# Kernel tuning notes

Hardware: AMD Instinct MI355X
Metric: run time of the kernel (lower is better)

## Reference

```python
import jax, jax.numpy as jnp
import numpy as np

D_MODEL = 1024
N_HEADS = 16
HEAD_DIM = D_MODEL // N_HEADS


def setup_inputs() -> dict:
    key = jax.random.key(0)
    ks = jax.random.split(key, 9)
    s = 1.0 / np.sqrt(D_MODEL)
    mk = lambda k: jax.random.uniform(k, (D_MODEL, D_MODEL), jnp.float32, -s, s)
    mb = lambda k: jax.random.uniform(k, (D_MODEL,), jnp.float32, -s, s)
    return {
        "x": jax.random.normal(ks[0], (2, 2048, D_MODEL), jnp.float32),
        "Wq": mk(ks[1]), "bq": mb(ks[2]),
        "Wk": mk(ks[3]), "bk": mb(ks[4]),
        "Wv": mk(ks[5]), "bv": mb(ks[6]),
        "Wo": mk(ks[7]), "bo": mb(ks[8]),
    }


def _split_heads(t, B, S):
    # [B,S,D] -> [B,H,S,hd]
    return t.reshape(B, S, N_HEADS, HEAD_DIM).transpose(0, 2, 1, 3)


def reference(x, Wq, bq, Wk, bk, Wv, bv, Wo, bo):
    B, S, _ = x.shape
    # torch Linear: y = x @ W.T + b  (W stored [out, in])
    Q = _split_heads(x @ Wq.T + bq, B, S)
    K = _split_heads(x @ Wk.T + bk, B, S)
    V = _split_heads(x @ Wv.T + bv, B, S)
    scores = jnp.einsum("bhsd,bhtd->bhst", Q, K) / np.sqrt(HEAD_DIM).astype(np.float32)
    attn = jax.nn.softmax(scores, axis=-1)
    out = jnp.einsum("bhst,bhtd->bhsd", attn, V)
    out = out.transpose(0, 2, 1, 3).reshape(B, S, D_MODEL)
    return out @ Wo.T + bo
```

## Files before the change

kernel.cpp:

```cpp
#include <hip/hip_runtime.h>
#include <math.h>

#define D_MODEL 1024
#define NH 16
#define HD 64
#define SEQ 2048
#define NB 2
#define BSROWS (NB * SEQ)
#define NT (SEQ / 64)

typedef __attribute__((ext_vector_type(8)))  short short8;
typedef __attribute__((ext_vector_type(4)))  float f32x4;
typedef __attribute__((ext_vector_type(16))) float f32x16;

__device__ __forceinline__ ushort bf16rne(float f) {
    union { float f; uint32_t u; } v; v.f = f;
    return (ushort)((v.u + 0x7FFFu + ((v.u >> 16) & 1u)) >> 16);
}

__device__ __forceinline__ void gl_lds16(const void* g, void* l) {
    __builtin_amdgcn_global_load_lds(
        reinterpret_cast<const uint32_t __attribute__((address_space(1)))*>(
            reinterpret_cast<uintptr_t>(g)),
        reinterpret_cast<uint32_t __attribute__((address_space(3)))*>(
            reinterpret_cast<uintptr_t>(l)),
        16, 0, 0);
}

__global__ __launch_bounds__(256) void convert_x(const float* __restrict__ in,
                                                 ushort* __restrict__ out) {
    const int i = blockIdx.x * 256 + threadIdx.x;
    const float4 a = ((const float4*)in)[2 * i];
    const float4 b = ((const float4*)in)[2 * i + 1];
    union { ushort u[8]; uint4 v; } r;
    r.u[0] = bf16rne(a.x); r.u[1] = bf16rne(a.y); r.u[2] = bf16rne(a.z); r.u[3] = bf16rne(a.w);
    r.u[4] = bf16rne(b.x); r.u[5] = bf16rne(b.y); r.u[6] = bf16rne(b.z); r.u[7] = bf16rne(b.w);
    ((uint4*)out)[i] = r.v;
}

__global__ __launch_bounds__(256) void convert_w(const float* __restrict__ w0,
                                                 const float* __restrict__ w1,
                                                 const float* __restrict__ w2,
                                                 const float* __restrict__ w3,
                                                 ushort* __restrict__ qkv,
                                                 ushort* __restrict__ wo) {
    const int which = blockIdx.y;
    const float* src = (which == 0) ? w0 : (which == 1) ? w1 : (which == 2) ? w2 : w3;
    ushort* dst = (which < 3) ? (qkv + (size_t)which * D_MODEL * D_MODEL) : wo;
    const int i = blockIdx.x * 256 + threadIdx.x;
    const float4 a = ((const float4*)src)[2 * i];
    const float4 b = ((const float4*)src)[2 * i + 1];
    union { ushort u[8]; uint4 v; } r;
    r.u[0] = bf16rne(a.x); r.u[1] = bf16rne(a.y); r.u[2] = bf16rne(a.z); r.u[3] = bf16rne(a.w);
    r.u[4] = bf16rne(b.x); r.u[5] = bf16rne(b.y); r.u[6] = bf16rne(b.z); r.u[7] = bf16rne(b.w);
    ((uint4*)dst)[i] = r.v;
}

template <int BN, int MODE>
__global__ __launch_bounds__(256) void gemm_mfma(const ushort* __restrict__ A,
                                                 const ushort* __restrict__ B,
                                                 const float* __restrict__ b0,
                                                 const float* __restrict__ b1,
                                                 const float* __restrict__ b2,
                                                 void* __restrict__ o0v,
                                                 void* __restrict__ o1v,
                                                 void* __restrict__ o2v) {
    constexpr int BM = 128, BK = 32;
    constexpr int WN = (BN == 128) ? 64 : 32;
    constexpr int NM = 4;
    constexpr int NN = WN / 16;

    __shared__ ushort As[BM * BK];
    __shared__ ushort Bs[BN * BK];

    const int tid = threadIdx.x;
    const int w   = tid >> 6;
    const int l   = tid & 63;
    const int i0  = blockIdx.x * BM;
    const int n0  = blockIdx.y * BN;

    const int wr = (w >> 1) * 64;
    const int wc = (w & 1) * WN;

    const int srow = l >> 2;
    const int scol = (l & 3) * 8;
    const ushort* ga = A + (size_t)(i0 + w * 32 + srow) * D_MODEL + scol;
    const ushort* gb = B + (size_t)(n0 + w * (BN / 4) + srow) * D_MODEL + scol;
    ushort* lA = &As[(w * 32) * BK];
    ushort* lB = &Bs[(w * (BN / 4)) * BK];

    f32x4 acc[NM][NN];
#pragma unroll
    for (int m = 0; m < NM; ++m)
#pragma unroll
        for (int n = 0; n < NN; ++n) acc[m][n] = (f32x4){0.f, 0.f, 0.f, 0.f};

    const int fr = l & 15;
    const int kc = (l >> 4) * 8;

    for (int k0 = 0; k0 < D_MODEL; k0 += BK) {
        __syncthreads();
        gl_lds16(ga, lA);
        gl_lds16(ga + 16 * D_MODEL, lA + 16 * BK);
        gl_lds16(gb, lB);
        if (BN == 128) gl_lds16(gb + 16 * D_MODEL, lB + 16 * BK);
        ga += BK; gb += BK;
        __syncthreads();

        short8 af[NM], bfr[NN];
#pragma unroll
        for (int m = 0; m < NM; ++m)
            af[m] = *(const short8*)&As[(wr + m * 16 + fr) * BK + kc];
#pragma unroll
        for (int n = 0; n < NN; ++n)
            bfr[n] = *(const short8*)&Bs[(wc + n * 16 + fr) * BK + kc];
#pragma unroll
        for (int m = 0; m < NM; ++m)
#pragma unroll
            for (int n = 0; n < NN; ++n)
                acc[m][n] = __builtin_amdgcn_mfma_f32_16x16x32_bf16(af[m], bfr[n], acc[m][n], 0, 0, 0);
    }

    const int rr = (l >> 4) * 4;

    if (MODE == 1) {
        float* out = (float*)o0v;
#pragma unroll
        for (int n = 0; n < NN; ++n) {
            const int j = n0 + wc + n * 16 + fr;
            const float bj = b0[j];
#pragma unroll
            for (int m = 0; m < NM; ++m) {
                const int row = i0 + wr + m * 16 + rr;
#pragma unroll
                for (int r = 0; r < 4; ++r)
                    out[(size_t)(row + r) * D_MODEL + j] = acc[m][n][r] + bj;
            }
        }
    } else {
        const int p = n0 >> 10;
        const float* bias = (p == 0) ? b0 : (p == 1) ? b1 : b2;
        const float scl = (p == 0) ? 0.125f : 1.0f;
#pragma unroll
        for (int n = 0; n < NN; ++n) {
            const int j = n0 + wc + n * 16 + fr;
            const int f = j & 1023;
            const float bj = bias[f];
            const int h = f >> 6, d = f & 63;
#pragma unroll
            for (int m = 0; m < NM; ++m) {
                const int row = i0 + wr + m * 16 + rr;
                const int bb = row >> 11;
                const int s0 = row & (SEQ - 1);
                if (p < 2) {
                    ushort* dst = (ushort*)(p == 0 ? o0v : o1v);
#pragma unroll
                    for (int r = 0; r < 4; ++r)
                        dst[(((size_t)bb * NH + h) * SEQ + (s0 + r)) * HD + d] =
                            bf16rne((acc[m][n][r] + bj) * scl);
                } else {
                    ushort4 pk;
                    pk.x = bf16rne(acc[m][n][0] + bj);
                    pk.y = bf16rne(acc[m][n][1] + bj);
                    pk.z = bf16rne(acc[m][n][2] + bj);
                    pk.w = bf16rne(acc[m][n][3] + bj);
                    *(ushort4*)&((ushort*)o2v)[(((size_t)bb * NH + h) * HD + d) * SEQ + s0] = pk;
                }
            }
        }
    }
}

__global__ __launch_bounds__(256) void attn_mfma3(const ushort* __restrict__ Q,
                                                  const ushort* __restrict__ K,
                                                  const ushort* __restrict__ Vt,
                                                  ushort* __restrict__ Aout) {
    __shared__ ushort KsB[2 * 4096];
    __shared__ ushort VtsB[2 * 4096];

    const int tid = threadIdx.x;
    const int w   = tid >> 6;
    const int l   = tid & 63;
    const int lq  = l & 31;
    const int hi  = l >> 5;
    const int qt  = blockIdx.x;
    const int h   = blockIdx.y;
    const int b   = blockIdx.z;
    const size_t bh = (size_t)b * NH + h;

    const ushort* Qg = Q  + (bh * SEQ + (size_t)qt * 128 + w * 32 + lq) * HD;
    const ushort* Kg = K  + bh * SEQ * HD;
    const ushort* Vg = Vt + bh * HD * SEQ;

    short8 qf[4];
#pragma unroll
    for (int dk = 0; dk < 4; ++dk)
        qf[dk] = *(const short8*)&Qg[dk * 16 + hi * 8];

    int srow[2], scol[2], ssw[2];
#pragma unroll
    for (int j = 0; j < 2; ++j) {
        const int idx = tid + j * 256;
        srow[j] = idx >> 3;
        scol[j] = (idx & 7) * 8;
        ssw[j]  = scol[j] ^ ((srow[j] & 7) << 3);
    }

    uint4 kreg[2], vreg[2];
#pragma unroll
    for (int j = 0; j < 2; ++j) {
        kreg[j] = *(const uint4*)&Kg[(size_t)srow[j] * HD + scol[j]];
        vreg[j] = *(const uint4*)&Vg[(size_t)srow[j] * SEQ + scol[j]];
    }
#pragma unroll
    for (int j = 0; j < 2; ++j) {
        *(uint4*)&KsB [srow[j] * 64 + ssw[j]] = kreg[j];
        *(uint4*)&VtsB[srow[j] * 64 + ssw[j]] = vreg[j];
    }
    __syncthreads();

    f32x16 oa0, oa1;
#pragma unroll
    for (int r = 0; r < 16; ++r) { oa0[r] = 0.f; oa1[r] = 0.f; }
    float m = -3.0e38f, lsum = 0.f;

    for (int kt = 0; kt < NT; ++kt) {
        const ushort* Ks  = &KsB [(kt & 1) * 4096];
        const ushort* Vts = &VtsB[(kt & 1) * 4096];
        ushort* Ksn  = &KsB [((kt + 1) & 1) * 4096];
        ushort* Vtsn = &VtsB[((kt + 1) & 1) * 4096];

        if (kt + 1 < NT) {
#pragma unroll
            for (int j = 0; j < 2; ++j) {
                kreg[j] = *(const uint4*)&Kg[((size_t)(kt + 1) * 64 + srow[j]) * HD + scol[j]];
                vreg[j] = *(const uint4*)&Vg[(size_t)srow[j] * SEQ + (kt + 1) * 64 + scol[j]];
            }
        }

        f32x16 sc0, sc1;
#pragma unroll
        for (int r = 0; r < 16; ++r) { sc0[r] = 0.f; sc1[r] = 0.f; }
        const int ksw0 = (lq & 7) << 3;
        __builtin_amdgcn_s_setprio(1);
#pragma unroll
        for (int dk = 0; dk < 4; ++dk) {
            const int col = (dk * 16 + hi * 8) ^ ksw0;
            const short8 kf0 = *(const short8*)&Ks[lq * 64 + col];
            const short8 kf1 = *(const short8*)&Ks[(32 + lq) * 64 + col];
            sc0 = __builtin_amdgcn_mfma_f32_32x32x16_bf16(kf0, qf[dk], sc0, 0, 0, 0);
            sc1 = __builtin_amdgcn_mfma_f32_32x32x16_bf16(kf1, qf[dk], sc1, 0, 0, 0);
        }
        __builtin_amdgcn_s_setprio(0);

        float t0 = fmaxf(fmaxf(sc0[0], sc0[1]), fmaxf(sc0[2], sc0[3]));
        float t1 = fmaxf(fmaxf(sc0[4], sc0[5]), fmaxf(sc0[6], sc0[7]));
        float t2 = fmaxf(fmaxf(sc0[8], sc0[9]), fmaxf(sc0[10], sc0[11]));
        float t3 = fmaxf(fmaxf(sc0[12], sc0[13]), fmaxf(sc0[14], sc0[15]));
        float u0 = fmaxf(fmaxf(sc1[0], sc1[1]), fmaxf(sc1[2], sc1[3]));
        float u1 = fmaxf(fmaxf(sc1[4], sc1[5]), fmaxf(sc1[6], sc1[7]));
        float u2 = fmaxf(fmaxf(sc1[8], sc1[9]), fmaxf(sc1[10], sc1[11]));
        float u3 = fmaxf(fmaxf(sc1[12], sc1[13]), fmaxf(sc1[14], sc1[15]));
        float pm = fmaxf(fmaxf(fmaxf(t0, t1), fmaxf(t2, t3)),
                         fmaxf(fmaxf(u0, u1), fmaxf(u2, u3)));
        pm = fmaxf(pm, __shfl_xor(pm, 32));

        if (!__all(pm - m <= 8.0f)) {
            const float mn = fmaxf(m, pm);
            const float corr = __expf(m - mn);
            m = mn; lsum *= corr;
#pragma unroll
            for (int r = 0; r < 16; ++r) { oa0[r] *= corr; oa1[r] *= corr; }
        }

        float p0[16], p1[16];
#pragma unroll
        for (int r = 0; r < 16; ++r) { p0[r] = __expf(sc0[r] - m); p1[r] = __expf(sc1[r] - m); }
        lsum += (((p0[0] + p0[1]) + (p0[2] + p0[3])) + ((p0[4] + p0[5]) + (p0[6] + p0[7])))
              + (((p0[8] + p0[9]) + (p0[10] + p0[11])) + ((p0[12] + p0[13]) + (p0[14] + p0[15])))
              + (((p1[0] + p1[1]) + (p1[2] + p1[3])) + ((p1[4] + p1[5]) + (p1[6] + p1[7])))
              + (((p1[8] + p1[9]) + (p1[10] + p1[11])) + ((p1[12] + p1[13]) + (p1[14] + p1[15])));

        uint32_t pk0[8], pk1[8], x0[8], x1[8];
#pragma unroll
        for (int i = 0; i < 8; ++i) {
            asm("v_cvt_pk_bf16_f32 %0, %1, %2" : "=v"(pk0[i]) : "v"(p0[2 * i]), "v"(p0[2 * i + 1]));
            asm("v_cvt_pk_bf16_f32 %0, %1, %2" : "=v"(pk1[i]) : "v"(p1[2 * i]), "v"(p1[2 * i + 1]));
        }
#pragma unroll
        for (int i = 0; i < 8; ++i) { x0[i] = __shfl_xor(pk0[i], 32); x1[i] = __shfl_xor(pk1[i], 32); }

        union U8 { uint32_t u[4]; short8 s; };
        U8 a0, a1, b0, b1;
        a0.u[0] = hi ? x0[2]  : pk0[0];  a0.u[1] = hi ? x0[3]  : pk0[1];
        a0.u[2] = hi ? pk0[2] : x0[0];   a0.u[3] = hi ? pk0[3] : x0[1];
        a1.u[0] = hi ? x0[6]  : pk0[4];  a1.u[1] = hi ? x0[7]  : pk0[5];
        a1.u[2] = hi ? pk0[6] : x0[4];   a1.u[3] = hi ? pk0[7] : x0[5];
        b0.u[0] = hi ? x1[2]  : pk1[0];  b0.u[1] = hi ? x1[3]  : pk1[1];
        b0.u[2] = hi ? pk1[2] : x1[0];   b0.u[3] = hi ? pk1[3] : x1[1];
        b1.u[0] = hi ? x1[6]  : pk1[4];  b1.u[1] = hi ? x1[7]  : pk1[5];
        b1.u[2] = hi ? pk1[6] : x1[4];   b1.u[3] = hi ? pk1[7] : x1[5];
        const short8 pf00 = a0.s, pf01 = a1.s, pf10 = b0.s, pf11 = b1.s;

        const int d0 = lq, d1 = 32 + lq;
        const int vsw0 = (d0 & 7) << 3;
        const int tA = hi * 8;
        const short8 vA0 = *(const short8*)&Vts[d0 * 64 + ((tA)      ^ vsw0)];
        const short8 vA1 = *(const short8*)&Vts[d1 * 64 + ((tA)      ^ vsw0)];
        const short8 vB0 = *(const short8*)&Vts[d0 * 64 + ((tA + 16) ^ vsw0)];
        const short8 vB1 = *(const short8*)&Vts[d1 * 64 + ((tA + 16) ^ vsw0)];
        const short8 wA0 = *(const short8*)&Vts[d0 * 64 + ((tA + 32) ^ vsw0)];
        const short8 wA1 = *(const short8*)&Vts[d1 * 64 + ((tA + 32) ^ vsw0)];
        const short8 wB0 = *(const short8*)&Vts[d0 * 64 + ((tA + 48) ^ vsw0)];
        const short8 wB1 = *(const short8*)&Vts[d1 * 64 + ((tA + 48) ^ vsw0)];
        __builtin_amdgcn_s_setprio(1);
        oa0 = __builtin_amdgcn_mfma_f32_32x32x16_bf16(vA0, pf00, oa0, 0, 0, 0);
        oa1 = __builtin_amdgcn_mfma_f32_32x32x16_bf16(vA1, pf00, oa1, 0, 0, 0);
        oa0 = __builtin_amdgcn_mfma_f32_32x32x16_bf16(vB0, pf01, oa0, 0, 0, 0);
        oa1 = __builtin_amdgcn_mfma_f32_32x32x16_bf16(vB1, pf01, oa1, 0, 0, 0);
        oa0 = __builtin_amdgcn_mfma_f32_32x32x16_bf16(wA0, pf10, oa0, 0, 0, 0);
        oa1 = __builtin_amdgcn_mfma_f32_32x32x16_bf16(wA1, pf10, oa1, 0, 0, 0);
        oa0 = __builtin_amdgcn_mfma_f32_32x32x16_bf16(wB0, pf11, oa0, 0, 0, 0);
        oa1 = __builtin_amdgcn_mfma_f32_32x32x16_bf16(wB1, pf11, oa1, 0, 0, 0);
        __builtin_amdgcn_s_setprio(0);

        if (kt + 1 < NT) {
#pragma unroll
            for (int j = 0; j < 2; ++j) {
                *(uint4*)&Ksn [srow[j] * 64 + ssw[j]] = kreg[j];
                *(uint4*)&Vtsn[srow[j] * 64 + ssw[j]] = vreg[j];
            }
        }
        __syncthreads();
    }

    lsum += __shfl_xor(lsum, 32);
    const float inv = 1.f / lsum;

    ushort* Ow = KsB + w * 2048;
#pragma unroll
    for (int r = 0; r < 16; ++r) {
        const int dd = (r & 3) + 8 * (r >> 2) + 4 * hi;
        const int swq = (lq & 7) << 3;
        Ow[lq * 64 + ((dd)      ^ swq)] = bf16rne(oa0[r] * inv);
        Ow[lq * 64 + ((dd + 32) ^ swq)] = bf16rne(oa1[r] * inv);
    }
    const size_t orow0 = (size_t)b * SEQ + (size_t)qt * 128 + w * 32;
#pragma unroll
    for (int i = 0; i < 4; ++i) {
        const int row = (l >> 3) + 8 * i;
        const int d0 = (l & 7) * 8;
        const uint4 v = *(const uint4*)&Ow[row * 64 + (d0 ^ ((row & 7) << 3))];
        *(uint4*)&Aout[(orow0 + row) * D_MODEL + h * HD + d0] = v;
    }
}

extern "C" void kernel_launch(void* const* d_in, const int* in_sizes, int n_in,
                              void* d_out, int out_size, void* d_ws, size_t ws_size,
                              hipStream_t stream) {
    const float* x  = (const float*)d_in[0];
    const float* Wq = (const float*)d_in[1];
    const float* bq = (const float*)d_in[2];
    const float* Wk = (const float*)d_in[3];
    const float* bk = (const float*)d_in[4];
    const float* Wv = (const float*)d_in[5];
    const float* bv = (const float*)d_in[6];
    const float* Wo = (const float*)d_in[7];
    const float* bo = (const float*)d_in[8];
    float* out = (float*)d_out;

    ushort* xb   = (ushort*)d_ws;
    ushort* Wqkv = xb   + (size_t)BSROWS * D_MODEL;
    ushort* Wob  = Wqkv + (size_t)3 * D_MODEL * D_MODEL;
    ushort* Qw   = Wob  + (size_t)D_MODEL * D_MODEL;
    ushort* Kw   = Qw   + (size_t)BSROWS * D_MODEL;
    ushort* Vw   = Kw   + (size_t)BSROWS * D_MODEL;
    ushort* Ab   = Vw   + (size_t)BSROWS * D_MODEL;

    convert_w<<<dim3(512, 4), 256, 0, stream>>>(Wq, Wk, Wv, Wo, Wqkv, Wob);
    convert_x<<<dim3(2048), 256, 0, stream>>>(x, xb);

    gemm_mfma<128, 0><<<dim3(32, 24), 256, 0, stream>>>(
        xb, Wqkv, bq, bk, bv, Qw, Kw, Vw);

    attn_mfma3<<<dim3(SEQ / 128, NH, NB), 256, 0, stream>>>(Qw, Kw, Vw, Ab);

    gemm_mfma<64, 1><<<dim3(32, 16), 256, 0, stream>>>(
        Ab, Wob, bo, nullptr, nullptr, out, nullptr, nullptr);
}
```

Baseline: 144.3 us.

## Merge conversion kernels, fold log2e into Q scale, widen output GEMM tile

The two fp32-to-bf16 conversion launches become one kernel with an 8-row grid, which removes one launch. The Q scale now includes log2(e), so softmax uses exp2f in place of __expf, and the rescale threshold is raised to match base-2 units. The output projection GEMM moves from BN=64 to BN=128, halving its grid to 256 blocks. The larger tile improves data reuse but may leave compute units underused on a large GPU.

```diff
diff --git a/kernel.cpp b/kernel.cpp
--- a/kernel.cpp
+++ b/kernel.cpp
@@ -27,27 +27,27 @@
         16, 0, 0);
 }
 
-__global__ __launch_bounds__(256) void convert_x(const float* __restrict__ in,
-                                                 ushort* __restrict__ out) {
-    const int i = blockIdx.x * 256 + threadIdx.x;
-    const float4 a = ((const float4*)in)[2 * i];
-    const float4 b = ((const float4*)in)[2 * i + 1];
-    union { ushort u[8]; uint4 v; } r;
-    r.u[0] = bf16rne(a.x); r.u[1] = bf16rne(a.y); r.u[2] = bf16rne(a.z); r.u[3] = bf16rne(a.w);
-    r.u[4] = bf16rne(b.x); r.u[5] = bf16rne(b.y); r.u[6] = bf16rne(b.z); r.u[7] = bf16rne(b.w);
-    ((uint4*)out)[i] = r.v;
-}
-
-__global__ __launch_bounds__(256) void convert_w(const float* __restrict__ w0,
-                                                 const float* __restrict__ w1,
-                                                 const float* __restrict__ w2,
-                                                 const float* __restrict__ w3,
-                                                 ushort* __restrict__ qkv,
-                                                 ushort* __restrict__ wo) {
+__global__ __launch_bounds__(256) void convert_all(const float* __restrict__ x,
+                                                   const float* __restrict__ w0,
+                                                   const float* __restrict__ w1,
+                                                   const float* __restrict__ w2,
+                                                   const float* __restrict__ w3,
+                                                   ushort* __restrict__ xb,
+                                                   ushort* __restrict__ qkv,
+                                                   ushort* __restrict__ wo) {
     const int which = blockIdx.y;
-    const float* src = (which == 0) ? w0 : (which == 1) ? w1 : (which == 2) ? w2 : w3;
-    ushort* dst = (which < 3) ? (qkv + (size_t)which * D_MODEL * D_MODEL) : wo;
-    const int i = blockIdx.x * 256 + threadIdx.x;
+    const float* src;
+    ushort* dst;
+    int i;
+    if (which < 4) {
+        src = (which == 0) ? w0 : (which == 1) ? w1 : (which == 2) ? w2 : w3;
+        dst = (which < 3) ? (qkv + (size_t)which * D_MODEL * D_MODEL) : wo;
+        i   = blockIdx.x * 256 + threadIdx.x;
+    } else {
+        src = x;
+        dst = xb;
+        i   = ((which - 4) * 512 + blockIdx.x) * 256 + threadIdx.x;
+    }
     const float4 a = ((const float4*)src)[2 * i];
     const float4 b = ((const float4*)src)[2 * i + 1];
     union { ushort u[8]; uint4 v; } r;
@@ -140,7 +140,7 @@
     } else {
         const int p = n0 >> 10;
         const float* bias = (p == 0) ? b0 : (p == 1) ? b1 : b2;
-        const float scl = (p == 0) ? 0.125f : 1.0f;
+        const float scl = (p == 0) ? 0.18033688011112042f : 1.0f;
 #pragma unroll
         for (int n = 0; n < NN; ++n) {
             const int j = n0 + wc + n * 16 + fr;
@@ -171,7 +171,7 @@
     }
 }
 
-__global__ __launch_bounds__(256) void attn_mfma3(const ushort* __restrict__ Q,
+__global__ __launch_bounds__(256) void attn_mfma6(const ushort* __restrict__ Q,
                                                   const ushort* __restrict__ K,
                                                   const ushort* __restrict__ Vt,
                                                   ushort* __restrict__ Aout) {
@@ -265,9 +265,9 @@
                          fmaxf(fmaxf(u0, u1), fmaxf(u2, u3)));
         pm = fmaxf(pm, __shfl_xor(pm, 32));
 
-        if (!__all(pm - m <= 8.0f)) {
+        if (!__all(pm - m <= 11.0f)) {
             const float mn = fmaxf(m, pm);
-            const float corr = __expf(m - mn);
+            const float corr = exp2f(m - mn);
             m = mn; lsum *= corr;
 #pragma unroll
             for (int r = 0; r < 16; ++r) { oa0[r] *= corr; oa1[r] *= corr; }
@@ -275,7 +275,7 @@
 
         float p0[16], p1[16];
 #pragma unroll
-        for (int r = 0; r < 16; ++r) { p0[r] = __expf(sc0[r] - m); p1[r] = __expf(sc1[r] - m); }
+        for (int r = 0; r < 16; ++r) { p0[r] = exp2f(sc0[r] - m); p1[r] = exp2f(sc1[r] - m); }
         lsum += (((p0[0] + p0[1]) + (p0[2] + p0[3])) + ((p0[4] + p0[5]) + (p0[6] + p0[7])))
               + (((p0[8] + p0[9]) + (p0[10] + p0[11])) + ((p0[12] + p0[13]) + (p0[14] + p0[15])))
               + (((p1[0] + p1[1]) + (p1[2] + p1[3])) + ((p1[4] + p1[5]) + (p1[6] + p1[7])))
@@ -377,14 +377,13 @@
     ushort* Vw   = Kw   + (size_t)BSROWS * D_MODEL;
     ushort* Ab   = Vw   + (size_t)BSROWS * D_MODEL;
 
-    convert_w<<<dim3(512, 4), 256, 0, stream>>>(Wq, Wk, Wv, Wo, Wqkv, Wob);
-    convert_x<<<dim3(2048), 256, 0, stream>>>(x, xb);
+    convert_all<<<dim3(512, 8), 256, 0, stream>>>(x, Wq, Wk, Wv, Wo, xb, Wqkv, Wob);
 
     gemm_mfma<128, 0><<<dim3(32, 24), 256, 0, stream>>>(
         xb, Wqkv, bq, bk, bv, Qw, Kw, Vw);
 
-    attn_mfma3<<<dim3(SEQ / 128, NH, NB), 256, 0, stream>>>(Qw, Kw, Vw, Ab);
-
-    gemm_mfma<64, 1><<<dim3(32, 16), 256, 0, stream>>>(
+    attn_mfma6<<<dim3(SEQ / 128, NH, NB), 256, 0, stream>>>(Qw, Kw, Vw, Ab);
+
+    gemm_mfma<128, 1><<<dim3(32, 8), 256, 0, stream>>>(
         Ab, Wob, bo, nullptr, nullptr, out, nullptr, nullptr);
 }
```

Result: slower. 156.5 us (+8.5%).
